# Performance work log

Measured on AMD Instinct MI355X. Metric: run time of the kernel, lower is better.

Reference implementation:

```python
import jax, jax.numpy as jnp
import numpy as np

U = 8          # units per modular layer
B = 16384      # batch
IN = 512       # input feature dim
H = 512        # modular hidden dim
NC = 62        # n_class


def _aggregate(P, h):
    # P: [T, F] policy link matrix; h: [F, B, D] per-unit features.
    # agg[t] = sum_f P[t,f] * h[f], normalized by row-sum when row-sum > 0.
    s = jnp.einsum('tf,fbd->tbd', P, h)
    row = P.sum(axis=1)                      # [T]
    safe = jnp.where(row > 0, row, 1.0)[:, None, None]
    return jnp.where((row > 0)[:, None, None], s / safe, s)


def setup_inputs() -> dict:
    key = jax.random.key(0)
    ks = jax.random.split(key, 12)
    s_in = 1.0 / np.sqrt(IN)
    s_h = 1.0 / np.sqrt(H)
    return {
        'x': jax.random.normal(ks[0], (B, IN), jnp.float32),
        'policy1': jax.random.uniform(ks[1], (U * U,), jnp.float32),
        'policy2': jax.random.uniform(ks[2], (U * U,), jnp.float32),
        'policy_final': jax.random.uniform(ks[3], (U,), jnp.float32),
        'W0': jax.random.uniform(ks[4], (U, IN, H), jnp.float32, -s_in, s_in),
        'b0': jax.random.uniform(ks[5], (U, H), jnp.float32, -s_in, s_in),
        'W1': jax.random.uniform(ks[6], (U, H, H), jnp.float32, -s_h, s_h),
        'b1': jax.random.uniform(ks[7], (U, H), jnp.float32, -s_h, s_h),
        'W2': jax.random.uniform(ks[8], (U, H, NC), jnp.float32, -s_h, s_h),
        'b2': jax.random.uniform(ks[9], (U, NC), jnp.float32, -s_h, s_h),
    }


def reference(x, policy1, policy2, policy_final, W0, b0, W1, b1, W2, b2):
    # Layer 0 (input modular layer): policy_list[0] is forced to all-ones,
    # so every unit sees x unscaled. Each unit: Linear + ReLU.
    h0 = jax.nn.relu(jnp.einsum('bi,uid->ubd', x, W0) + b0[:, None, :])  # [U,B,H]

    # Mid layer: policy-gated weighted-sum aggregation, then per-unit Linear+ReLU.
    a1 = _aggregate(policy1.reshape(U, U), h0)
    h1 = jax.nn.relu(jnp.einsum('ubi,uid->ubd', a1, W1) + b1[:, None, :])

    # Output modular layer: aggregate then per-unit Linear (no activation).
    a2 = _aggregate(policy2.reshape(U, U), h1)
    h2 = jnp.einsum('ubi,uic->ubc', a2, W2) + b2[:, None, :]  # [U,B,NC]

    # Final gating. Original code divides by divider INSIDE the unit loop
    # (every iteration), so replicate that recurrence exactly.
    d = policy_final.sum()
    inv = jnp.where(d > 0, 1.0 / jnp.where(d > 0, d, 1.0), 1.0)
    out = jnp.zeros((B, NC), jnp.float32)
    for j in range(U):  # fixed small unit count, not a data dim
        out = (out + h2[j] * policy_final[j]) * inv
    return out
```

## Files before the change

kernel.cpp:

```cpp
#include <hip/hip_runtime.h>

#define U_   8
#define B_   16384
#define NC_  62

typedef __attribute__((ext_vector_type(8))) short bfrag;
typedef __attribute__((ext_vector_type(4))) float facc;

__device__ __forceinline__ float bf2f(unsigned int lo16) {
    union { unsigned int i; float f; } v;
    v.i = lo16 << 16;
    return v.f;
}
__device__ __forceinline__ unsigned short f2bf(float f) {
    unsigned int x = __float_as_uint(f);
    return (unsigned short)((x + 0x7fffu + ((x >> 16) & 1u)) >> 16);
}
__device__ __forceinline__ void gl2lds16(const void* g, void* l) {
    __builtin_amdgcn_global_load_lds(
        (const __attribute__((address_space(1))) void*)g,
        (__attribute__((address_space(3))) void*)l, 16, 0, 0);
}

__global__ void prep_kernel(const float* __restrict__ p1, const float* __restrict__ p2,
                            const float* __restrict__ pf, const float* __restrict__ b2,
                            float* __restrict__ P1n, float* __restrict__ P2n,
                            float* __restrict__ wfin, float* __restrict__ cconst)
{
    int t = threadIdx.x;
    if (t >= 64) return;
    int row = t >> 3;
    float s1 = 0.f, s2 = 0.f;
    for (int f = 0; f < 8; f++) { s1 += p1[row * 8 + f]; s2 += p2[row * 8 + f]; }
    P1n[t] = p1[t] * (s1 > 0.f ? 1.f / s1 : 1.f);
    P2n[t] = p2[t] * (s2 > 0.f ? 1.f / s2 : 1.f);
    float d = 0.f;
    for (int j = 0; j < 8; j++) d += pf[j];
    float inv = d > 0.f ? 1.f / d : 1.f;
    float wv[8];
    for (int j = 0; j < 8; j++) {
        float v = pf[j];
        for (int i = j; i < 8; i++) v *= inv;
        wv[j] = v;
    }
    if (t < 8) wfin[t] = wv[t];
    float cc = 0.f;
    if (t < NC_) for (int u = 0; u < 8; u++) cc += wv[u] * b2[u * NC_ + t];
    cconst[t] = cc;
}

__global__ __launch_bounds__(256) void mega_prep(
    const float* __restrict__ W0, unsigned short* __restrict__ W0r,
    const float* __restrict__ W1, unsigned short* __restrict__ W1t,
    const float* __restrict__ x, unsigned short* __restrict__ xb)
{
    __shared__ float tile[32][33];
    const int b = blockIdx.x;
    if (b < 4096) {
        const int bb = b & 2047;
        const int u  = bb >> 8;
        const int n0 = (bb & 15) * 32, k0 = ((bb >> 4) & 15) * 32;
        const int tx = threadIdx.x & 31, ty = threadIdx.x >> 5;
        const float* Wb = (b < 2048 ? W0 : W1) + (long)u * 512 * 512;
#pragma unroll
        for (int i = 0; i < 4; i++)
            tile[ty + i * 8][tx] = Wb[(long)(k0 + ty + i * 8) * 512 + n0 + tx];
        __syncthreads();
        if (b < 2048) {
#pragma unroll
            for (int i = 0; i < 4; i++) {
                int n = n0 + ty + i * 8, k = k0 + tx;
                int np = (n >> 5) * 256 + u * 32 + (n & 31);
                W0r[(long)np * 512 + k] = f2bf(tile[tx][ty + i * 8]);
            }
        } else {
            unsigned short* Wo = W1t + (long)u * 512 * 512;
#pragma unroll
            for (int i = 0; i < 4; i++) {
                int n = n0 + ty + i * 8, k = k0 + tx;
                Wo[(long)n * 512 + k] = f2bf(tile[tx][ty + i * 8]);
            }
        }
    } else {
        long i = ((long)(b - 4096) * 256 + threadIdx.x) * 8;
        const float4* xp = (const float4*)(x + i);
        float4 a = xp[0], c = xp[1];
        uint4 o;
        o.x = f2bf(a.x) | ((unsigned)f2bf(a.y) << 16);
        o.y = f2bf(a.z) | ((unsigned)f2bf(a.w) << 16);
        o.z = f2bf(c.x) | ((unsigned)f2bf(c.y) << 16);
        o.w = f2bf(c.z) | ((unsigned)f2bf(c.w) << 16);
        *(uint4*)(xb + i) = o;
    }
}

__global__ __launch_bounds__(256) void wout_build(
    const float* __restrict__ W2, const float* __restrict__ P2n,
    const float* __restrict__ wfin, unsigned short* __restrict__ Woutt)
{
    const int c   = threadIdx.x & 63;
    const int row = blockIdx.x * 4 + (threadIdx.x >> 6);
    const int f = row >> 9, k = row & 511;
    float s = 0.f;
    if (c < NC_) {
#pragma unroll
        for (int u = 0; u < 8; u++)
            s += wfin[u] * P2n[u * 8 + f] * W2[((long)u * 512 + k) * NC_ + c];
    }
    Woutt[(long)c * 4096 + row] = f2bf(s);
}

__global__ __launch_bounds__(512, 4) void gemm0_mix(
    const unsigned short* __restrict__ xb, const unsigned short* __restrict__ W0r,
    const float* __restrict__ b0, const float* __restrict__ P1n,
    unsigned short* __restrict__ a1, long plane)
{
    __shared__ __align__(16) unsigned short sm[128 * 264];
    unsigned short* sA = sm;
    unsigned short* sB = sm + 128 * 64;
    const int tid = threadIdx.x, w = tid >> 6, lane = tid & 63;
    const int flat = blockIdx.x;
    const int xcd = flat & 7, seq = flat >> 3;
    const int ng = xcd * 2 + (seq & 1);
    const long mBase = (long)(seq >> 1) * 128;

    const int lr = lane >> 3;
    const int lg = (lane & 7) ^ lr;
    const int wm = w >> 2, wn = w & 3;
    const int r = lane & 15, q = lane >> 4;
    const int x7 = r & 7;

    facc acc[4][4];
#pragma unroll
    for (int i = 0; i < 4; i++)
#pragma unroll
        for (int j = 0; j < 4; j++) acc[i][j] = (facc){0.f, 0.f, 0.f, 0.f};

    for (int k0 = 0; k0 < 512; k0 += 64) {
        __syncthreads();
#pragma unroll
        for (int i = 0; i < 2; i++) {
            const int c = w + i * 8;
            gl2lds16(xb + (mBase + c * 8 + lr) * 512 + k0 + lg * 8, sA + c * 512);
        }
#pragma unroll
        for (int i = 0; i < 4; i++) {
            const int c = w * 4 + i;
            gl2lds16(W0r + ((long)ng * 256 + c * 8 + lr) * 512 + k0 + lg * 8,
                     sB + c * 512);
        }
        __syncthreads();
#pragma unroll
        for (int h = 0; h < 2; h++) {
            const int xg = ((h * 4 + q) ^ x7) * 8;
            bfrag aF[4], bF[4];
#pragma unroll
            for (int mt = 0; mt < 4; mt++)
                aF[mt] = *(const bfrag*)&sA[(wm * 64 + mt * 16 + r) * 64 + xg];
#pragma unroll
            for (int nt = 0; nt < 4; nt++)
                bF[nt] = *(const bfrag*)&sB[(wn * 64 + nt * 16 + r) * 64 + xg];
#pragma unroll
            for (int mt = 0; mt < 4; mt++)
#pragma unroll
                for (int nt = 0; nt < 4; nt++)
                    acc[mt][nt] = __builtin_amdgcn_mfma_f32_16x16x32_bf16(
                        aF[mt], bF[nt], acc[mt][nt], 0, 0, 0);
        }
    }

    __syncthreads();
#pragma unroll
    for (int nt = 0; nt < 4; nt++) {
        const int cl = wn * 64 + nt * 16 + r;
        const float bv = b0[(cl >> 5) * 512 + ng * 32 + (cl & 31)];
#pragma unroll
        for (int mt = 0; mt < 4; mt++) {
            const int rowb = wm * 64 + mt * 16 + q * 4;
#pragma unroll
            for (int rg = 0; rg < 4; rg++) {
                float v = acc[mt][nt][rg] + bv;
                v = v > 0.f ? v : 0.f;
                sm[(rowb + rg) * 264 + cl] = f2bf(v);
            }
        }
    }
    __syncthreads();

    float pw[64];
#pragma unroll
    for (int i = 0; i < 64; i++) pw[i] = P1n[i];
    const int row = tid >> 2, fs = (tid & 3) * 8;
    float hv[8][8];
#pragma unroll
    for (int u = 0; u < 8; u++) {
        bfrag hx = *(const bfrag*)&sm[row * 264 + u * 32 + fs];
#pragma unroll
        for (int j = 0; j < 8; j++)
            hv[u][j] = bf2f((unsigned int)(unsigned short)hx[j]);
    }
    const long rowOff = (mBase + row) * 512 + ng * 32 + fs;
#pragma unroll
    for (int t = 0; t < 8; t++) {
        float o[8];
#pragma unroll
        for (int j = 0; j < 8; j++) {
            float s = 0.f;
#pragma unroll
            for (int u = 0; u < 8; u++) s = fmaf(pw[t * 8 + u], hv[u][j], s);
            o[j] = s;
        }
        uint4 ov;
        ov.x = f2bf(o[0]) | ((unsigned)f2bf(o[1]) << 16);
        ov.y = f2bf(o[2]) | ((unsigned)f2bf(o[3]) << 16);
        ov.z = f2bf(o[4]) | ((unsigned)f2bf(o[5]) << 16);
        ov.w = f2bf(o[6]) | ((unsigned)f2bf(o[7]) << 16);
        *(uint4*)(a1 + (long)t * plane + rowOff) = ov;
    }
}

__global__ __launch_bounds__(512, 4) void gemm_h_out(
    const unsigned short* __restrict__ a1,
    const unsigned short* __restrict__ W1t,
    const float* __restrict__ b1,
    const unsigned short* __restrict__ Woutt,
    float* __restrict__ partial, long plane, int Bc)
{
    __shared__ __align__(16) unsigned short sm[32768];
    unsigned short* sA = sm;
    unsigned short* sB = sm + 16384;
    unsigned short* sH = sm;

    const int tid = threadIdx.x, w = tid >> 6, lane = tid & 63;
    const int flat = blockIdx.x;
    const int u = flat & 7;
    const int nb = (flat >> 3) & 3;
    const long mBase = (long)(flat >> 5) * 256;
    const int nBase = nb * 128;

    const int lr = lane >> 3, lg = (lane & 7) ^ lr;
    const int wm = w >> 1, wn = w & 1;
    const int r = lane & 15, q = lane >> 4;
    const int x7 = r & 7;

    const unsigned short* Ab = a1 + (long)u * plane;

    facc acc1[4][4];
#pragma unroll
    for (int i = 0; i < 4; i++)
#pragma unroll
        for (int j = 0; j < 4; j++) acc1[i][j] = (facc){0.f, 0.f, 0.f, 0.f};

    for (int k0 = 0; k0 < 512; k0 += 64) {
        __syncthreads();
#pragma unroll
        for (int i = 0; i < 4; i++) {
            const int c = w * 4 + i;
            gl2lds16(Ab + (mBase + c * 8 + lr) * 512 + k0 + lg * 8, sA + c * 512);
        }
#pragma unroll
        for (int i = 0; i < 2; i++) {
            const int c = w * 2 + i;
            gl2lds16(W1t + ((long)u * 512 + nBase + c * 8 + lr) * 512 + k0 + lg * 8,
                     sB + c * 512);
        }
        __syncthreads();
#pragma unroll
        for (int h = 0; h < 2; h++) {
            const int xg = ((h * 4 + q) ^ x7) * 8;
            bfrag aF[4], bF[4];
#pragma unroll
            for (int mt = 0; mt < 4; mt++)
                aF[mt] = *(const bfrag*)&sA[(wm * 64 + mt * 16 + r) * 64 + xg];
#pragma unroll
            for (int nt = 0; nt < 4; nt++)
                bF[nt] = *(const bfrag*)&sB[(wn * 64 + nt * 16 + r) * 64 + xg];
#pragma unroll
            for (int mt = 0; mt < 4; mt++)
#pragma unroll
                for (int nt = 0; nt < 4; nt++)
                    acc1[mt][nt] = __builtin_amdgcn_mfma_f32_16x16x32_bf16(
                        aF[mt], bF[nt], acc1[mt][nt], 0, 0, 0);
        }
    }

    __syncthreads();

#pragma unroll
    for (int nt = 0; nt < 4; nt++) {
        const int col = wn * 64 + nt * 16 + r;
        const float bv = b1[u * 512 + nBase + col];
        const int slab = col >> 6, cg = (col >> 3) & 7, ce = col & 7;
#pragma unroll
        for (int mt = 0; mt < 4; mt++) {
            const int rowb = wm * 64 + mt * 16 + q * 4;
#pragma unroll
            for (int rg = 0; rg < 4; rg++) {
                const int row = rowb + rg;
                float v = acc1[mt][nt][rg] + bv;
                v = v > 0.f ? v : 0.f;
                sH[slab * 16384 + row * 64 + ((cg ^ (row & 7)) * 8) + ce] = f2bf(v);
            }
        }
    }
    __syncthreads();

    facc acc2[2][4];
#pragma unroll
    for (int i = 0; i < 2; i++)
#pragma unroll
        for (int j = 0; j < 4; j++) acc2[i][j] = (facc){0.f, 0.f, 0.f, 0.f};

#pragma unroll
    for (int ks = 0; ks < 4; ks++) {
        const int kh = ks >> 1, h2 = ks & 1;
        bfrag aF2[2], bF2[4];
#pragma unroll
        for (int mt = 0; mt < 2; mt++) {
            const int row = w * 32 + mt * 16 + r;
            aF2[mt] = *(const bfrag*)&sH[kh * 16384 + row * 64
                                         + (((h2 * 4 + q) ^ x7) * 8)];
        }
#pragma unroll
        for (int nt = 0; nt < 4; nt++) {
            const int c = nt * 16 + r;
            bF2[nt] = *(const bfrag*)(Woutt + (long)c * 4096 + u * 512
                                      + nBase + ks * 32 + q * 8);
        }
#pragma unroll
        for (int mt = 0; mt < 2; mt++)
#pragma unroll
            for (int nt = 0; nt < 4; nt++)
                acc2[mt][nt] = __builtin_amdgcn_mfma_f32_16x16x32_bf16(
                    aF2[mt], bF2[nt], acc2[mt][nt], 0, 0, 0);
    }

    float* pb = partial + (((long)(u * 4 + nb)) * Bc + mBase) * 64;
#pragma unroll
    for (int nt = 0; nt < 4; nt++) {
        const int col = nt * 16 + r;
#pragma unroll
        for (int mt = 0; mt < 2; mt++) {
#pragma unroll
            for (int rg = 0; rg < 4; rg++) {
                const int row = w * 32 + mt * 16 + q * 4 + rg;
                pb[(long)row * 64 + col] = acc2[mt][nt][rg];
            }
        }
    }
}

__global__ __launch_bounds__(256) void reduce_out(
    const float* __restrict__ partial, const float* __restrict__ cconst,
    float* __restrict__ out, int Bc)
{
    const long flat = (long)blockIdx.x * 256 + threadIdx.x;
    const long row = flat >> 2;
    const int cg = (int)(flat & 3) * 16;
    float s[16];
#pragma unroll
    for (int j = 0; j < 16; j++) s[j] = 0.f;
    for (int p = 0; p < 32; p++) {
        const float4* pp = (const float4*)(partial + ((long)p * Bc + row) * 64 + cg);
#pragma unroll
        for (int v4 = 0; v4 < 4; v4++) {
            float4 v = pp[v4];
            s[v4 * 4 + 0] += v.x; s[v4 * 4 + 1] += v.y;
            s[v4 * 4 + 2] += v.z; s[v4 * 4 + 3] += v.w;
        }
    }
#pragma unroll
    for (int j = 0; j < 16; j++) {
        const int c = cg + j;
        if (c < NC_) out[row * NC_ + c] = s[j] + cconst[c];
    }
}

extern "C" void kernel_launch(void* const* d_in, const int* in_sizes, int n_in,
                              void* d_out, int out_size, void* d_ws, size_t ws_size,
                              hipStream_t stream)
{
    const float* x  = (const float*)d_in[0];
    const float* p1 = (const float*)d_in[1];
    const float* p2 = (const float*)d_in[2];
    const float* pf = (const float*)d_in[3];
    const float* W0 = (const float*)d_in[4];
    const float* b0 = (const float*)d_in[5];
    const float* W1 = (const float*)d_in[6];
    const float* b1 = (const float*)d_in[7];
    const float* W2 = (const float*)d_in[8];
    const float* b2 = (const float*)d_in[9];
    float* out = (float*)d_out;

    char* ws = (char*)d_ws;
    size_t off = 0;
    auto alloc = [&](size_t bytes) -> void* {
        void* p = ws + off;
        off += (bytes + 255) & ~(size_t)255;
        return p;
    };
    float* P1n    = (float*)alloc(64 * sizeof(float));
    float* P2n    = (float*)alloc(64 * sizeof(float));
    float* wfin   = (float*)alloc(8 * sizeof(float));
    float* cconst = (float*)alloc(64 * sizeof(float));
    unsigned short* W0r   = (unsigned short*)alloc((size_t)4096 * 512 * 2);
    unsigned short* W1t   = (unsigned short*)alloc((size_t)U_ * 512 * 512 * 2);
    unsigned short* Woutt = (unsigned short*)alloc((size_t)64 * 4096 * 2);
    unsigned short* xb    = (unsigned short*)alloc((size_t)B_ * 512 * 2);

    size_t remain = ws_size > off ? ws_size - off : 0;
    int Bc = 2048;
    for (int cand = B_; cand >= 2048; cand >>= 1) {
        size_t need = 8ull * cand * 512 * 2 + 32ull * cand * 64 * 4 + 1024;
        if (need <= remain) { Bc = cand; break; }
    }
    unsigned short* a1 = (unsigned short*)alloc(8ull * Bc * 512 * 2);
    float* partial     = (float*)alloc(32ull * Bc * 64 * 4);

    prep_kernel<<<1, 64, 0, stream>>>(p1, p2, pf, b2, P1n, P2n, wfin, cconst);
    mega_prep<<<dim3(8192), 256, 0, stream>>>(W0, W0r, W1, W1t, x, xb);
    wout_build<<<dim3(1024), 256, 0, stream>>>(W2, P2n, wfin, Woutt);

    const int Mb = Bc / 128;
    const int Mb2 = Bc / 256;
    const long plane = (long)Bc * 512;
    for (int bb = 0; bb < B_; bb += Bc) {
        gemm0_mix<<<dim3(16 * Mb), 512, 0, stream>>>(
            xb + (long)bb * 512, W0r, b0, P1n, a1, plane);
        gemm_h_out<<<dim3(32 * Mb2), 512, 0, stream>>>(
            a1, W1t, b1, Woutt, partial, plane, Bc);
        reduce_out<<<dim3(Bc / 64), 256, 0, stream>>>(
            partial, cconst, out + (long)bb * NC_, Bc);
    }
}
```

Before: 339.0 us.

## Loop two N-blocks per gemm_h_out block and fuse reduction into next gemm0 launch

gemm_h_out now processes two 128-column N-blocks inside each block, accumulating the output projection in registers. This halves the partial buffer to 16 planes and halves the reduction traffic. The reduction for the previous batch chunk is folded into the next gemm0_mix launch as extra tail blocks, and a single reduce_out runs only for the last chunk. This removes per-chunk launches and partial writes, at the cost of half as many gemm_h_out blocks (less parallelism). It also relies on the partial buffer being read before gemm_h_out overwrites it, which stream ordering guarantees.

New measurement: 627.1 us. +85.0%, slower.

```diff
diff --git a/kernel.cpp b/kernel.cpp
--- a/kernel.cpp
+++ b/kernel.cpp
@@ -113,9 +113,35 @@
 __global__ __launch_bounds__(512, 4) void gemm0_mix(
     const unsigned short* __restrict__ xb, const unsigned short* __restrict__ W0r,
     const float* __restrict__ b0, const float* __restrict__ P1n,
-    unsigned short* __restrict__ a1, long plane)
+    unsigned short* __restrict__ a1, long plane,
+    const float* __restrict__ partialPrev, const float* __restrict__ cconst,
+    float* __restrict__ outPrev, int gemmBlocks, int Bc)
 {
     __shared__ __align__(16) unsigned short sm[128 * 264];
+    if ((int)blockIdx.x >= gemmBlocks) {
+        const long flat2 = (long)(blockIdx.x - gemmBlocks) * 512 + threadIdx.x;
+        const long row = flat2 >> 2;
+        const int cg = (int)(flat2 & 3) * 16;
+        float s[16];
+#pragma unroll
+        for (int j = 0; j < 16; j++) s[j] = 0.f;
+        for (int p = 0; p < 16; p++) {
+            const float4* pp = (const float4*)(partialPrev + ((long)p * Bc + row) * 64 + cg);
+#pragma unroll
+            for (int v4 = 0; v4 < 4; v4++) {
+                float4 v = pp[v4];
+                s[v4 * 4 + 0] += v.x; s[v4 * 4 + 1] += v.y;
+                s[v4 * 4 + 2] += v.z; s[v4 * 4 + 3] += v.w;
+            }
+        }
+#pragma unroll
+        for (int j = 0; j < 16; j++) {
+            const int c = cg + j;
+            if (c < NC_) outPrev[row * NC_ + c] = s[j] + cconst[c];
+        }
+        return;
+    }
+
     unsigned short* sA = sm;
     unsigned short* sB = sm + 128 * 64;
     const int tid = threadIdx.x, w = tid >> 6, lane = tid & 63;
@@ -234,9 +260,8 @@
     const int tid = threadIdx.x, w = tid >> 6, lane = tid & 63;
     const int flat = blockIdx.x;
     const int u = flat & 7;
-    const int nb = (flat >> 3) & 3;
-    const long mBase = (long)(flat >> 5) * 256;
-    const int nBase = nb * 128;
+    const int nbo = (flat >> 3) & 1;
+    const long mBase = (long)(flat >> 4) * 256;
 
     const int lr = lane >> 3, lg = (lane & 7) ^ lr;
     const int wm = w >> 1, wn = w & 1;
@@ -245,97 +270,101 @@
 
     const unsigned short* Ab = a1 + (long)u * plane;
 
-    facc acc1[4][4];
-#pragma unroll
-    for (int i = 0; i < 4; i++)
-#pragma unroll
-        for (int j = 0; j < 4; j++) acc1[i][j] = (facc){0.f, 0.f, 0.f, 0.f};
-
-    for (int k0 = 0; k0 < 512; k0 += 64) {
+    facc acc2[2][4];
+#pragma unroll
+    for (int i = 0; i < 2; i++)
+#pragma unroll
+        for (int j = 0; j < 4; j++) acc2[i][j] = (facc){0.f, 0.f, 0.f, 0.f};
+
+    for (int nbi = 0; nbi < 2; nbi++) {
+        const int nBase = (nbo * 2 + nbi) * 128;
+
+        facc acc1[4][4];
+#pragma unroll
+        for (int i = 0; i < 4; i++)
+#pragma unroll
+            for (int j = 0; j < 4; j++) acc1[i][j] = (facc){0.f, 0.f, 0.f, 0.f};
+
+        for (int k0 = 0; k0 < 512; k0 += 64) {
+            __syncthreads();
+#pragma unroll
+            for (int i = 0; i < 4; i++) {
+                const int c = w * 4 + i;
+                gl2lds16(Ab + (mBase + c * 8 + lr) * 512 + k0 + lg * 8, sA + c * 512);
+            }
+#pragma unroll
+            for (int i = 0; i < 2; i++) {
+                const int c = w * 2 + i;
+                gl2lds16(W1t + ((long)u * 512 + nBase + c * 8 + lr) * 512 + k0 + lg * 8,
+                         sB + c * 512);
+            }
+            __syncthreads();
+#pragma unroll
+            for (int h = 0; h < 2; h++) {
+                const int xg = ((h * 4 + q) ^ x7) * 8;
+                bfrag aF[4], bF[4];
+#pragma unroll
+                for (int mt = 0; mt < 4; mt++)
+                    aF[mt] = *(const bfrag*)&sA[(wm * 64 + mt * 16 + r) * 64 + xg];
+#pragma unroll
+                for (int nt = 0; nt < 4; nt++)
+                    bF[nt] = *(const bfrag*)&sB[(wn * 64 + nt * 16 + r) * 64 + xg];
+#pragma unroll
+                for (int mt = 0; mt < 4; mt++)
+#pragma unroll
+                    for (int nt = 0; nt < 4; nt++)
+                        acc1[mt][nt] = __builtin_amdgcn_mfma_f32_16x16x32_bf16(
+                            aF[mt], bF[nt], acc1[mt][nt], 0, 0, 0);
+            }
+        }
+
         __syncthreads();
-#pragma unroll
-        for (int i = 0; i < 4; i++) {
-            const int c = w * 4 + i;
-            gl2lds16(Ab + (mBase + c * 8 + lr) * 512 + k0 + lg * 8, sA + c * 512);
-        }
-#pragma unroll
-        for (int i = 0; i < 2; i++) {
-            const int c = w * 2 + i;
-            gl2lds16(W1t + ((long)u * 512 + nBase + c * 8 + lr) * 512 + k0 + lg * 8,
-                     sB + c * 512);
+
+#pragma unroll
+        for (int nt = 0; nt < 4; nt++) {
+            const int col = wn * 64 + nt * 16 + r;
+            const float bv = b1[u * 512 + nBase + col];
+            const int slab = col >> 6, cg = (col >> 3) & 7, ce = col & 7;
+#pragma unroll
+            for (int mt = 0; mt < 4; mt++) {
+                const int rowb = wm * 64 + mt * 16 + q * 4;
+#pragma unroll
+                for (int rg = 0; rg < 4; rg++) {
+                    const int row = rowb + rg;
+                    float v = acc1[mt][nt][rg] + bv;
+                    v = v > 0.f ? v : 0.f;
+                    sH[slab * 16384 + row * 64 + ((cg ^ (row & 7)) * 8) + ce] = f2bf(v);
+                }
+            }
         }
         __syncthreads();
-#pragma unroll
-        for (int h = 0; h < 2; h++) {
-            const int xg = ((h * 4 + q) ^ x7) * 8;
-            bfrag aF[4], bF[4];
-#pragma unroll
-            for (int mt = 0; mt < 4; mt++)
-                aF[mt] = *(const bfrag*)&sA[(wm * 64 + mt * 16 + r) * 64 + xg];
-#pragma unroll
-            for (int nt = 0; nt < 4; nt++)
-                bF[nt] = *(const bfrag*)&sB[(wn * 64 + nt * 16 + r) * 64 + xg];
-#pragma unroll
-            for (int mt = 0; mt < 4; mt++)
+
+#pragma unroll
+        for (int ks = 0; ks < 4; ks++) {
+            const int kh = ks >> 1, h2 = ks & 1;
+            bfrag aF2[2], bF2[4];
+#pragma unroll
+            for (int mt = 0; mt < 2; mt++) {
+                const int row = w * 32 + mt * 16 + r;
+                aF2[mt] = *(const bfrag*)&sH[kh * 16384 + row * 64
+                                             + (((h2 * 4 + q) ^ x7) * 8)];
+            }
+#pragma unroll
+            for (int nt = 0; nt < 4; nt++) {
+                const int c = nt * 16 + r;
+                bF2[nt] = *(const bfrag*)(Woutt + (long)c * 4096 + u * 512
+                                          + nBase + ks * 32 + q * 8);
+            }
+#pragma unroll
+            for (int mt = 0; mt < 2; mt++)
 #pragma unroll
                 for (int nt = 0; nt < 4; nt++)
-                    acc1[mt][nt] = __builtin_amdgcn_mfma_f32_16x16x32_bf16(
-                        aF[mt], bF[nt], acc1[mt][nt], 0, 0, 0);
-        }
-    }
-
-    __syncthreads();
-
-#pragma unroll
-    for (int nt = 0; nt < 4; nt++) {
-        const int col = wn * 64 + nt * 16 + r;
-        const float bv = b1[u * 512 + nBase + col];
-        const int slab = col >> 6, cg = (col >> 3) & 7, ce = col & 7;
-#pragma unroll
-        for (int mt = 0; mt < 4; mt++) {
-            const int rowb = wm * 64 + mt * 16 + q * 4;
-#pragma unroll
-            for (int rg = 0; rg < 4; rg++) {
-                const int row = rowb + rg;
-                float v = acc1[mt][nt][rg] + bv;
-                v = v > 0.f ? v : 0.f;
-                sH[slab * 16384 + row * 64 + ((cg ^ (row & 7)) * 8) + ce] = f2bf(v);
-            }
-        }
-    }
-    __syncthreads();
-
-    facc acc2[2][4];
-#pragma unroll
-    for (int i = 0; i < 2; i++)
-#pragma unroll
-        for (int j = 0; j < 4; j++) acc2[i][j] = (facc){0.f, 0.f, 0.f, 0.f};
-
-#pragma unroll
-    for (int ks = 0; ks < 4; ks++) {
-        const int kh = ks >> 1, h2 = ks & 1;
-        bfrag aF2[2], bF2[4];
-#pragma unroll
-        for (int mt = 0; mt < 2; mt++) {
-            const int row = w * 32 + mt * 16 + r;
-            aF2[mt] = *(const bfrag*)&sH[kh * 16384 + row * 64
-                                         + (((h2 * 4 + q) ^ x7) * 8)];
-        }
-#pragma unroll
-        for (int nt = 0; nt < 4; nt++) {
-            const int c = nt * 16 + r;
-            bF2[nt] = *(const bfrag*)(Woutt + (long)c * 4096 + u * 512
-                                      + nBase + ks * 32 + q * 8);
-        }
-#pragma unroll
-        for (int mt = 0; mt < 2; mt++)
-#pragma unroll
-            for (int nt = 0; nt < 4; nt++)
-                acc2[mt][nt] = __builtin_amdgcn_mfma_f32_16x16x32_bf16(
-                    aF2[mt], bF2[nt], acc2[mt][nt], 0, 0, 0);
-    }
-
-    float* pb = partial + (((long)(u * 4 + nb)) * Bc + mBase) * 64;
+                    acc2[mt][nt] = __builtin_amdgcn_mfma_f32_16x16x32_bf16(
+                        aF2[mt], bF2[nt], acc2[mt][nt], 0, 0, 0);
+        }
+    }
+
+    float* pb = partial + (((long)(u * 2 + nbo)) * Bc + mBase) * 64;
 #pragma unroll
     for (int nt = 0; nt < 4; nt++) {
         const int col = nt * 16 + r;
@@ -350,17 +379,17 @@
     }
 }
 
-__global__ __launch_bounds__(256) void reduce_out(
+__global__ __launch_bounds__(512) void reduce_out(
     const float* __restrict__ partial, const float* __restrict__ cconst,
     float* __restrict__ out, int Bc)
 {
-    const long flat = (long)blockIdx.x * 256 + threadIdx.x;
+    const long flat = (long)blockIdx.x * 512 + threadIdx.x;
     const long row = flat >> 2;
     const int cg = (int)(flat & 3) * 16;
     float s[16];
 #pragma unroll
     for (int j = 0; j < 16; j++) s[j] = 0.f;
-    for (int p = 0; p < 32; p++) {
+    for (int p = 0; p < 16; p++) {
         const float4* pp = (const float4*)(partial + ((long)p * Bc + row) * 64 + cg);
 #pragma unroll
         for (int v4 = 0; v4 < 4; v4++) {
@@ -411,25 +440,28 @@
     size_t remain = ws_size > off ? ws_size - off : 0;
     int Bc = 2048;
     for (int cand = B_; cand >= 2048; cand >>= 1) {
-        size_t need = 8ull * cand * 512 * 2 + 32ull * cand * 64 * 4 + 1024;
+        size_t need = 12288ull * cand + 1024;
         if (need <= remain) { Bc = cand; break; }
     }
     unsigned short* a1 = (unsigned short*)alloc(8ull * Bc * 512 * 2);
-    float* partial     = (float*)alloc(32ull * Bc * 64 * 4);
+    float* partial     = (float*)alloc(16ull * Bc * 64 * 4);
 
     prep_kernel<<<1, 64, 0, stream>>>(p1, p2, pf, b2, P1n, P2n, wfin, cconst);
     mega_prep<<<dim3(8192), 256, 0, stream>>>(W0, W0r, W1, W1t, x, xb);
     wout_build<<<dim3(1024), 256, 0, stream>>>(W2, P2n, wfin, Woutt);
 
     const int Mb = Bc / 128;
-    const int Mb2 = Bc / 256;
+    const int gemmBlocks = 16 * Mb;
     const long plane = (long)Bc * 512;
     for (int bb = 0; bb < B_; bb += Bc) {
-        gemm0_mix<<<dim3(16 * Mb), 512, 0, stream>>>(
-            xb + (long)bb * 512, W0r, b0, P1n, a1, plane);
-        gemm_h_out<<<dim3(32 * Mb2), 512, 0, stream>>>(
+        const int extra = (bb > 0) ? Bc / 128 : 0;
+        float* outPrev = (bb > 0) ? out + (long)(bb - Bc) * NC_ : nullptr;
+        gemm0_mix<<<dim3(gemmBlocks + extra), 512, 0, stream>>>(
+            xb + (long)bb * 512, W0r, b0, P1n, a1, plane,
+            partial, cconst, outPrev, gemmBlocks, Bc);
+        gemm_h_out<<<dim3(16 * (Bc / 256)), 512, 0, stream>>>(
             a1, W1t, b1, Woutt, partial, plane, Bc);
-        reduce_out<<<dim3(Bc / 64), 256, 0, stream>>>(
-            partial, cconst, out + (long)bb * NC_, Bc);
-    }
-}
+    }
+    reduce_out<<<dim3(Bc / 128), 512, 0, stream>>>(
+        partial, cconst, out + (long)(B_ - Bc) * NC_, Bc);
+}
```
